# Kernel optimization log

Measured on AMD Instinct MI355X. Metric: run time of the kernel, lower is better.

The kernel has to match this reference:

```python
import jax, jax.numpy as jnp
import numpy as np

D_MODEL = 96
D_INNER = 2 * D_MODEL          # expand=2
D_STATE = 16
D_CONV = 4
DT_RANK = 6                    # ceil(96/16)


def setup_inputs() -> dict:
    key = jax.random.key(0)
    ks = jax.random.split(key, 12)
    B, C, H, W = 4, D_MODEL, 64, 64
    # dt_proj bias init (inverse-softplus of dt sampled log-uniform in [1e-3, 1e-1])
    dtv = jnp.exp(jax.random.uniform(ks[7], (D_INNER,), jnp.float32)
                  * (np.log(0.1) - np.log(0.001)) + np.log(0.001))
    dtv = jnp.clip(dtv, 1e-4, None)
    dt_proj_b = dtv + jnp.log(-jnp.expm1(-dtv))
    dt_std = DT_RANK ** -0.5
    return {
        "x": jax.random.normal(ks[0], (B, C, H, W), jnp.float32),
        "proj_w": jax.random.normal(ks[1], (2 * C, C, 1, 1), jnp.float32) * 0.05,
        "dconv_w": jax.random.normal(ks[2], (C, 2 * C, 3, 3), jnp.float32) * 0.02,
        "in_proj_w": jax.random.normal(ks[3], (2 * D_INNER, C), jnp.float32) * 0.05,
        "conv1d_w": jax.random.normal(ks[4], (D_INNER, D_CONV), jnp.float32) * 0.2,
        "conv1d_b": jnp.zeros((D_INNER,), jnp.float32),
        "x_proj_w": jax.random.normal(ks[5], (DT_RANK + 2 * D_STATE, D_INNER), jnp.float32) * 0.05,
        "dt_proj_w": jax.random.uniform(ks[6], (D_INNER, DT_RANK), jnp.float32, -dt_std, dt_std),
        "dt_proj_b": dt_proj_b,
        "A_log": jnp.log(jnp.tile(jnp.arange(1, D_STATE + 1, dtype=jnp.float32), (D_INNER, 1))),
        "D": jnp.ones((D_INNER,), jnp.float32),
        "out_proj_w": jax.random.normal(ks[8], (C, D_INNER), jnp.float32) * 0.05,
    }


def _cssm_forward(x, proj_w, dconv_w, in_proj_w, conv1d_w, conv1d_b,
                  x_proj_w, dt_proj_w, dt_proj_b, A_log, D, out_proj_w):
    Bsz, Cdim, H, W = x.shape
    L = H * W
    # proj (1x1 conv, no bias) then dconv (3x3 conv, pad 1, no bias)
    xp = jax.lax.conv_general_dilated(x, proj_w, (1, 1), 'VALID',
                                      dimension_numbers=('NCHW', 'OIHW', 'NCHW'))
    xp = jax.lax.conv_general_dilated(xp, dconv_w, (1, 1), ((1, 1), (1, 1)),
                                      dimension_numbers=('NCHW', 'OIHW', 'NCHW'))
    seq = xp.reshape(Bsz, Cdim, L).transpose(0, 2, 1)            # (B, L, C)
    # in_proj (no bias) -> (B, 2*d_inner, L)
    xz = jnp.einsum('blc,ec->bel', seq, in_proj_w)
    xin, z = jnp.split(xz, 2, axis=1)                             # (B, d_inner, L) each
    # causal depthwise conv1d (pad d_conv-1 on left) + SiLU
    xpad = jnp.pad(xin, ((0, 0), (0, 0), (D_CONV - 1, 0)))
    xc = jax.lax.conv_general_dilated(xpad, conv1d_w[:, None, :], (1,), 'VALID',
                                      dimension_numbers=('NCH', 'OIH', 'NCH'),
                                      feature_group_count=D_INNER)
    xc = jax.nn.silu(xc + conv1d_b[None, :, None])                # (B, d_inner, L)
    # x_proj -> dt (rank), B (state), C (state)
    x_dbl = jnp.einsum('bdl,ed->ble', xc, x_proj_w)               # (B, L, rank+2n)
    dt, Bc, Cc = jnp.split(x_dbl, [DT_RANK, DT_RANK + D_STATE], axis=-1)
    delta = jax.nn.softplus(jnp.einsum('blr,dr->bld', dt, dt_proj_w) + dt_proj_b)  # (B,L,d)
    A = -jnp.exp(A_log)                                           # (d, n)
    u = xc.transpose(0, 2, 1)                                     # (B, L, d)
    # selective scan: h_t = exp(delta_t A) * h_{t-1} + delta_t B_t u_t  (diag, per channel/state)
    dA = jnp.exp(delta[..., None] * A)                            # (B,L,d,n)
    dBu = delta[..., None] * Bc[:, :, None, :] * u[..., None]     # (B,L,d,n)

    def combine(c1, c2):
        a1, b1 = c1
        a2, b2 = c2
        return a2 * a1, a2 * b1 + b2

    _, h = jax.lax.associative_scan(combine, (dA, dBu), axis=1)   # (B,L,d,n)
    y = jnp.einsum('bldn,bln->bld', h, Cc) + D * u                # (B,L,d)
    y = y * jax.nn.silu(z.transpose(0, 2, 1))                     # gate
    out = jnp.einsum('bld,cd->blc', y, out_proj_w)                # (B,L,C)
    return out.transpose(0, 2, 1).reshape(Bsz, Cdim, H, W)


def reference(x, proj_w, dconv_w, in_proj_w, conv1d_w, conv1d_b,
              x_proj_w, dt_proj_w, dt_proj_b, A_log, D, out_proj_w):
    return _cssm_forward(x, proj_w, dconv_w, in_proj_w, conv1d_w, conv1d_b,
                         x_proj_w, dt_proj_w, dt_proj_b, A_log, D, out_proj_w)
```

## Files before the change

kernel.cpp:

```cpp
#include <hip/hip_runtime.h>
#include <math.h>

#define LL    4096
#define CDIM  96
#define DIN   192
#define NST   16
#define XE    38

typedef __attribute__((ext_vector_type(8))) short v8s;
typedef __attribute__((ext_vector_type(4))) float v4f;
typedef unsigned short ushort_t;
typedef unsigned int uint_t;

#if __has_builtin(__builtin_amdgcn_exp2f)
__device__ __forceinline__ float fexp2(float x) { return __builtin_amdgcn_exp2f(x); }
#else
__device__ __forceinline__ float fexp2(float x) { return exp2f(x); }
#endif
#if __has_builtin(__builtin_amdgcn_logf)
__device__ __forceinline__ float flog2(float x) { return __builtin_amdgcn_logf(x); }
#else
__device__ __forceinline__ float flog2(float x) { return __log2f(x); }
#endif

__device__ __forceinline__ float siluf(float x) {
    return x * __builtin_amdgcn_rcpf(1.f + fexp2(-1.44269504f * x));
}
__device__ __forceinline__ ushort_t f2bf(float f) {
    uint_t u = __builtin_bit_cast(uint_t, f);
    return (ushort_t)((u + 0x7fffu + ((u >> 16) & 1u)) >> 16);
}
__device__ __forceinline__ float bf2f(ushort_t u) {
    return __builtin_bit_cast(float, (uint_t)u << 16);
}

__global__ __launch_bounds__(256) void k_prep(const float* __restrict__ proj_w,
                                              const float* __restrict__ dconv_w,
                                              const float* __restrict__ in_proj_w,
                                              const float* __restrict__ out_proj_w,
                                              const float* __restrict__ x_proj_w,
                                              const float* __restrict__ x,
                                              ushort_t* __restrict__ Wbf,
                                              ushort_t* __restrict__ Wibf,
                                              ushort_t* __restrict__ Wobf,
                                              ushort_t* __restrict__ Wxbf,
                                              ushort_t* __restrict__ xT) {
    int bid = blockIdx.x;
    if (bid < 576) {
        int i = bid * 256 + threadIdx.x;
        if (i < 82944) {
            int k = i % 9;
            int c = (i / 9) % 96;
            int o = i / 864;
            float s = 0.f;
            for (int j = 0; j < 192; ++j)
                s += dconv_w[(o * 192 + j) * 9 + k] * proj_w[j * 96 + c];
            Wbf[(k * 96 + o) * 96 + c] = f2bf(s);
            return;
        }
        i -= 82944;
        if (i < 36864) { Wibf[i] = f2bf(in_proj_w[i]); return; }
        i -= 36864;
        if (i < 18432) { Wobf[i] = f2bf(out_proj_w[i]); return; }
        i -= 18432;
        if (i < 9216) {
            int e = i / 192;
            Wxbf[i] = (e < XE) ? f2bf(x_proj_w[i]) : (ushort_t)0;
        }
        return;
    }
    int bid2 = bid - 576;
    int yy = bid2 % 66;
    int b  = bid2 / 66;
    int yv = yy - 1;
    for (int i = threadIdx.x; i < 68 * 12; i += 256) {
        int xx = i % 68, cig = i / 68;
        int xv = xx - 1;
        ushort_t u[8];
        if (yv >= 0 && yv < 64 && xv >= 0 && xv < 64) {
            const float* sp = x + ((size_t)(b * 96 + cig * 8)) * LL + yv * 64 + xv;
#pragma unroll
            for (int j = 0; j < 8; ++j) u[j] = f2bf(sp[j * LL]);
        } else {
#pragma unroll
            for (int j = 0; j < 8; ++j) u[j] = 0;
        }
        uint4 pk;
        pk.x = u[0] | ((uint_t)u[1] << 16); pk.y = u[2] | ((uint_t)u[3] << 16);
        pk.z = u[4] | ((uint_t)u[5] << 16); pk.w = u[6] | ((uint_t)u[7] << 16);
        *(uint4*)(xT + (((size_t)b * 66 + yy) * 68 + xx) * 96 + cig * 8) = pk;
    }
}

__global__ __launch_bounds__(384, 2) void k_convin(const ushort_t* __restrict__ xT,
                                                   const ushort_t* __restrict__ Wbf,
                                                   const ushort_t* __restrict__ Wibf,
                                                   ushort_t* __restrict__ xzb) {
    __shared__ ushort_t s_seq[32 * 104];
    int tid = threadIdx.x;
    int w = tid >> 6, l = tid & 63;
    int n = l & 15, g = l >> 4;
    int blk = blockIdx.x;
    int b = blk >> 7, rem = blk & 127;
    int y = rem >> 1, half = rem & 1;
    int lx = (w & 1) * 16;
    int x0 = half * 32 + lx;
    int co0 = (w >> 1) * 32;
    v4f acc0 = {0.f, 0.f, 0.f, 0.f};
    v4f acc1 = {0.f, 0.f, 0.f, 0.f};
    const ushort_t* xb = xT + (((size_t)b * 66 + y) * 68 + x0 + n) * 96 + g * 8;
    const ushort_t* aw = Wbf + ((size_t)co0 + n) * 96 + g * 8;
#pragma unroll
    for (int tap = 0; tap < 9; ++tap) {
        int dy = tap / 3, dx = tap % 3;
        const ushort_t* bp = xb + (dy * 68 + dx) * 96;
        const ushort_t* ap = aw + (size_t)tap * 9216;
#pragma unroll
        for (int kk = 0; kk < 3; ++kk) {
            v8s bf = *(const v8s*)(bp + kk * 32);
            v8s a0 = *(const v8s*)(ap + kk * 32);
            v8s a1 = *(const v8s*)(ap + 1536 + kk * 32);
            acc0 = __builtin_amdgcn_mfma_f32_16x16x32_bf16(a0, bf, acc0, 0, 0, 0);
            acc1 = __builtin_amdgcn_mfma_f32_16x16x32_bf16(a1, bf, acc1, 0, 0, 0);
        }
    }
    {
        int ll = lx + n;
        ushort_t* sp = s_seq + ll * 104 + co0 + g * 4;
        ushort4 p0, p1;
        p0.x = f2bf(acc0[0]); p0.y = f2bf(acc0[1]); p0.z = f2bf(acc0[2]); p0.w = f2bf(acc0[3]);
        p1.x = f2bf(acc1[0]); p1.y = f2bf(acc1[1]); p1.z = f2bf(acc1[2]); p1.w = f2bf(acc1[3]);
        *(ushort4*)sp = p0;
        *(ushort4*)(sp + 16) = p1;
    }
    __syncthreads();
    int coh = w * 64;
    v4f acc[4][2];
#pragma unroll
    for (int mt = 0; mt < 4; ++mt)
#pragma unroll
        for (int lt = 0; lt < 2; ++lt) acc[mt][lt] = (v4f){0.f, 0.f, 0.f, 0.f};
    const ushort_t* ap2 = Wibf + ((size_t)coh + n) * 96 + g * 8;
#pragma unroll
    for (int lt = 0; lt < 2; ++lt) {
        const ushort_t* bp2 = s_seq + (lt * 16 + n) * 104 + g * 8;
#pragma unroll
        for (int kk = 0; kk < 3; ++kk) {
            v8s bf = *(const v8s*)(bp2 + kk * 32);
#pragma unroll
            for (int mt = 0; mt < 4; ++mt) {
                v8s af = *(const v8s*)(ap2 + mt * 16 * 96 + kk * 32);
                acc[mt][lt] = __builtin_amdgcn_mfma_f32_16x16x32_bf16(af, bf, acc[mt][lt], 0, 0, 0);
            }
        }
    }
    int l0g = y * 64 + half * 32;
    ushort_t* ob = xzb + (size_t)b * 384 * LL + l0g + n;
#pragma unroll
    for (int mt = 0; mt < 4; ++mt) {
        int e = coh + mt * 16 + g * 4;
#pragma unroll
        for (int lt = 0; lt < 2; ++lt)
#pragma unroll
            for (int r = 0; r < 4; ++r)
                ob[(size_t)(e + r) * LL + lt * 16] = f2bf(acc[mt][lt][r]);
    }
}

__global__ __launch_bounds__(256) void k_conv1d(const ushort_t* __restrict__ xzb,
                                                const float* __restrict__ w,
                                                const float* __restrict__ bias,
                                                ushort_t* __restrict__ xcT) {
    int tid = threadIdx.x;
    int d_l = tid >> 2, tg = tid & 3;
    int b = blockIdx.z, dg = blockIdx.y, tt = blockIdx.x;
    int d = dg * 64 + d_l;
    int t0 = tt * 16 + tg * 4;
    const ushort_t* xin = xzb + (size_t)(b * 384 + d) * LL;
    ushort4 cu = *(const ushort4*)(xin + t0);
    float pm3 = 0.f, pm2 = 0.f, pm1 = 0.f;
    if (t0 > 0) {
        ushort4 pv = *(const ushort4*)(xin + t0 - 4);
        pm3 = bf2f(pv.y); pm2 = bf2f(pv.z); pm1 = bf2f(pv.w);
    }
    float in[7] = {pm3, pm2, pm1, bf2f(cu.x), bf2f(cu.y), bf2f(cu.z), bf2f(cu.w)};
    float w0 = w[d * 4 + 0], w1 = w[d * 4 + 1], w2 = w[d * 4 + 2], w3 = w[d * 4 + 3];
    float bb = bias[d];
    ushort_t* xt = xcT + ((size_t)b * 4096 + t0) * DIN + d;
#pragma unroll
    for (int i = 0; i < 4; ++i) {
        float s = bb + w0 * in[i] + w1 * in[i + 1] + w2 * in[i + 2] + w3 * in[i + 3];
        xt[(size_t)i * DIN] = f2bf(siluf(s));
    }
}

__global__ __launch_bounds__(256, 4) void k_xprojm(const ushort_t* __restrict__ xcT,
                                                   const ushort_t* __restrict__ Wxbf,
                                                   float* __restrict__ dtT,
                                                   float* __restrict__ BtP,
                                                   float* __restrict__ CtP) {
    int tid = threadIdx.x;
    int w = tid >> 6, l = tid & 63;
    int n = l & 15, g = l >> 4;
    int b = blockIdx.y;
    int l0 = blockIdx.x * 64 + w * 16;
    const ushort_t* bp = xcT + ((size_t)b * 4096 + l0 + n) * 192 + g * 8;
    const ushort_t* ap = Wxbf + (size_t)n * 192 + g * 8;
    v4f acc[3];
#pragma unroll
    for (int m = 0; m < 3; ++m) acc[m] = (v4f){0.f, 0.f, 0.f, 0.f};
#pragma unroll
    for (int kk = 0; kk < 6; ++kk) {
        v8s bf = *(const v8s*)(bp + kk * 32);
#pragma unroll
        for (int m = 0; m < 3; ++m) {
            v8s af = *(const v8s*)(ap + m * 16 * 192 + kk * 32);
            acc[m] = __builtin_amdgcn_mfma_f32_16x16x32_bf16(af, bf, acc[m], 0, 0, 0);
        }
    }
    float* dtb = dtT + (size_t)b * 6 * LL + l0 + n;
    float* Bb = BtP + ((size_t)b * LL + l0 + n) * 16;
    float* Cb = CtP + ((size_t)b * LL + l0 + n) * 16;
#pragma unroll
    for (int m = 0; m < 3; ++m)
#pragma unroll
        for (int r = 0; r < 4; ++r) {
            int e = m * 16 + g * 4 + r;
            float v = acc[m][r];
            if (e < 6)       dtb[(size_t)e * LL] = v;
            else if (e < 22) Bb[e - 6] = v;
            else if (e < 38) Cb[e - 22] = v;
        }
}

__global__ __launch_bounds__(512, 6) void k_scan(const float* __restrict__ dtT,
                                                 const float* __restrict__ dtw,
                                                 const float* __restrict__ dtpb,
                                                 const float* __restrict__ c1w,
                                                 const float* __restrict__ c1b,
                                                 const float* __restrict__ BtP,
                                                 const float* __restrict__ CtP,
                                                 const float* __restrict__ A_log,
                                                 const float* __restrict__ Dp,
                                                 ushort_t* __restrict__ xzb) {
    __shared__ float s_d[32 * 132];
    __shared__ float s_u[32 * 132];
    __shared__ float s_a[32][17];
    __shared__ float s_h[32][17];
    int tid = threadIdx.x;
    int n = tid & 15, cg = tid >> 4;
    int bd = blockIdx.x;
    int d = bd % DIN, b = bd / DIN;
    const ushort_t* xin  = xzb + (size_t)(b * 384 + d) * LL;
    const ushort_t* zrow = xzb + (size_t)(b * 384 + DIN + d) * LL;
    ushort_t* ygr = xzb + (size_t)(b * 384 + d) * LL;
    float A2 = -__expf(A_log[d * NST + n]) * 1.44269504f;
    float Dd = Dp[d];

    {
        int t8 = tid * 8;
        int li = ((t8 >> 7) * 132) + (t8 & 127);
        float ee[11];
        if (t8 > 0) {
            ushort4 pv = *(const ushort4*)(xin + t8 - 4);
            ee[0] = bf2f(pv.y); ee[1] = bf2f(pv.z); ee[2] = bf2f(pv.w);
        } else {
            ee[0] = ee[1] = ee[2] = 0.f;
        }
        v8s cu = *(const v8s*)(xin + t8);
#pragma unroll
        for (int j = 0; j < 8; ++j) ee[3 + j] = bf2f((ushort_t)cu[j]);
        float cw0 = c1w[d * 4], cw1 = c1w[d * 4 + 1], cw2 = c1w[d * 4 + 2], cw3 = c1w[d * 4 + 3];
        float cb = c1b[d];
#pragma unroll
        for (int j = 0; j < 8; ++j) {
            float s = cb + cw0 * ee[j] + cw1 * ee[j + 1] + cw2 * ee[j + 2] + cw3 * ee[j + 3];
            s_u[li + j] = siluf(s);
        }
        const float* dt0 = dtT + (size_t)b * 6 * LL + t8;
        const float* wr = dtw + d * 6;
        float w0 = wr[0], w1 = wr[1], w2 = wr[2], w3 = wr[3], w4 = wr[4], w5 = wr[5];
        float bb = dtpb[d];
        {
            v4f ra[6];
#pragma unroll
            for (int r = 0; r < 6; ++r) ra[r] = *(const v4f*)(dt0 + r * LL);
            v4f spa;
#pragma unroll
            for (int j = 0; j < 4; ++j) {
                float s1 = bb + w0 * ra[0][j] + w1 * ra[1][j] + w2 * ra[2][j]
                              + w3 * ra[3][j] + w4 * ra[4][j] + w5 * ra[5][j];
                spa[j] = 0.69314718f * flog2(1.f + fexp2(s1 * 1.44269504f));
            }
            *(v4f*)&s_d[li] = spa;
        }
        {
            v4f rb[6];
#pragma unroll
            for (int r = 0; r < 6; ++r) rb[r] = *(const v4f*)(dt0 + r * LL + 4);
            v4f spb;
#pragma unroll
            for (int j = 0; j < 4; ++j) {
                float s2 = bb + w0 * rb[0][j] + w1 * rb[1][j] + w2 * rb[2][j]
                              + w3 * rb[3][j] + w4 * rb[4][j] + w5 * rb[5][j];
                spb[j] = 0.69314718f * flog2(1.f + fexp2(s2 * 1.44269504f));
            }
            *(v4f*)&s_d[li + 4] = spb;
        }
    }
    __syncthreads();

    int t0 = cg * 128;
    int lb = cg * 132;
    const float* pB = BtP + ((size_t)b * LL + t0) * 16 + n;
    const float* pC = CtP + ((size_t)b * LL + t0) * 16 + n;

    float h = 0.f, sdu = 0.f;
    float4 du_c = *(float4*)&s_d[lb];
    float4 u_c  = *(float4*)&s_u[lb];
    float B0 = pB[0], B1 = pB[16], B2 = pB[32], B3 = pB[48];
    for (int s = 0; s < 31; ++s) {
        int ln = lb + s * 4 + 4;
        const float* pBn = pB + s * 64 + 64;
        float4 du_n = *(float4*)&s_d[ln];
        float4 u_n  = *(float4*)&s_u[ln];
        float Bn0 = pBn[0], Bn1 = pBn[16], Bn2 = pBn[32], Bn3 = pBn[48];
        float a0 = fexp2(du_c.x * A2), a1 = fexp2(du_c.y * A2);
        float a2 = fexp2(du_c.z * A2), a3 = fexp2(du_c.w * A2);
        h = fmaf(a0, h, (du_c.x * u_c.x) * B0);
        h = fmaf(a1, h, (du_c.y * u_c.y) * B1);
        h = fmaf(a2, h, (du_c.z * u_c.z) * B2);
        h = fmaf(a3, h, (du_c.w * u_c.w) * B3);
        sdu += (du_c.x + du_c.y) + (du_c.z + du_c.w);
        du_c = du_n; u_c = u_n; B0 = Bn0; B1 = Bn1; B2 = Bn2; B3 = Bn3;
    }
    {
        float a0 = fexp2(du_c.x * A2), a1 = fexp2(du_c.y * A2);
        float a2 = fexp2(du_c.z * A2), a3 = fexp2(du_c.w * A2);
        h = fmaf(a0, h, (du_c.x * u_c.x) * B0);
        h = fmaf(a1, h, (du_c.y * u_c.y) * B1);
        h = fmaf(a2, h, (du_c.z * u_c.z) * B2);
        h = fmaf(a3, h, (du_c.w * u_c.w) * B3);
        sdu += (du_c.x + du_c.y) + (du_c.z + du_c.w);
    }
    s_a[cg][n] = fexp2(sdu * A2);
    s_h[cg][n] = h;
    __syncthreads();

    {
        int l = tid & 63, w = tid >> 6;
        int c = l & 31, nn = (w << 1) | (l >> 5);
        float a  = s_a[c][nn];
        float hh = s_h[c][nn];
#pragma unroll
        for (int st = 1; st < 32; st <<= 1) {
            float ap = __shfl_up(a, st, 32);
            float hp = __shfl_up(hh, st, 32);
            bool ok = (c >= st);
            hh = ok ? fmaf(a, hp, hh) : hh;
            a  = ok ? a * ap : a;
        }
        float h0 = __shfl_up(hh, 1, 32);
        if (c == 0) h0 = 0.f;
        s_a[c][nn] = h0;
    }
    __syncthreads();

    h = s_a[cg][n];
    const int j = n & 3;
    const bool e1 = (j == 1), e2 = (j == 2), e3 = (j == 3);
    du_c = *(float4*)&s_d[lb];
    u_c  = *(float4*)&s_u[lb];
    B0 = pB[0]; B1 = pB[16]; B2 = pB[32]; B3 = pB[48];
    float C0 = pC[0], C1 = pC[16], C2 = pC[32], C3 = pC[48];
    ushort4 z_c = *(const ushort4*)(zrow + t0);
    for (int s = 0; s < 32; ++s) {
        float4 du_n, u_n;
        ushort4 z_n;
        float Bn0, Bn1, Bn2, Bn3, Cn0, Cn1, Cn2, Cn3;
        if (s < 31) {
            int ln = lb + s * 4 + 4;
            const float* pBn = pB + s * 64 + 64;
            const float* pCn = pC + s * 64 + 64;
            du_n = *(float4*)&s_d[ln];
            u_n  = *(float4*)&s_u[ln];
            Bn0 = pBn[0]; Bn1 = pBn[16]; Bn2 = pBn[32]; Bn3 = pBn[48];
            Cn0 = pCn[0]; Cn1 = pCn[16]; Cn2 = pCn[32]; Cn3 = pCn[48];
            z_n = *(const ushort4*)(zrow + t0 + s * 4 + 4);
        }
        float a0 = fexp2(du_c.x * A2), a1 = fexp2(du_c.y * A2);
        float a2 = fexp2(du_c.z * A2), a3 = fexp2(du_c.w * A2);
        h = fmaf(a0, h, (du_c.x * u_c.x) * B0); float p0 = h * C0;
        h = fmaf(a1, h, (du_c.y * u_c.y) * B1); float p1 = h * C1;
        h = fmaf(a2, h, (du_c.z * u_c.z) * B2); float p2 = h * C2;
        h = fmaf(a3, h, (du_c.w * u_c.w) * B3); float p3 = h * C3;
        p0 += __shfl_xor(p0, 1); p0 += __shfl_xor(p0, 2);
        p1 += __shfl_xor(p1, 1); p1 += __shfl_xor(p1, 2);
        p2 += __shfl_xor(p2, 1); p2 += __shfl_xor(p2, 2);
        p3 += __shfl_xor(p3, 1); p3 += __shfl_xor(p3, 2);
        float pj = e3 ? p3 : (e2 ? p2 : (e1 ? p1 : p0));
        pj += __shfl_xor(pj, 4); pj += __shfl_xor(pj, 8);
        float uj = e3 ? u_c.w : (e2 ? u_c.z : (e1 ? u_c.y : u_c.x));
        ushort_t zu = e3 ? z_c.w : (e2 ? z_c.z : (e1 ? z_c.y : z_c.x));
        float yj = fmaf(Dd, uj, pj) * siluf(bf2f(zu));
        if (n < 4)
            ygr[t0 + s * 4 + n] = f2bf(yj);
        du_c = du_n; u_c = u_n; z_c = z_n;
        B0 = Bn0; B1 = Bn1; B2 = Bn2; B3 = Bn3;
        C0 = Cn0; C1 = Cn1; C2 = Cn2; C3 = Cn3;
    }
}

__global__ __launch_bounds__(384, 6) void k_outproj(const ushort_t* __restrict__ xzb,
                                                    const ushort_t* __restrict__ Wobf,
                                                    float* __restrict__ out) {
    __shared__ ushort_t s_yg[16][232];
    int tid = threadIdx.x;
    int b = blockIdx.y;
    int l0 = blockIdx.x * 16;
    const ushort_t* ygb = xzb + (size_t)b * 384 * LL;
    if (tid < 96) {
        int q = tid >> 1, o = tid & 1;
        uint4 v[4];
#pragma unroll
        for (int jj = 0; jj < 4; ++jj)
            v[jj] = *(const uint4*)(ygb + (size_t)(q * 4 + jj) * LL + l0 + o * 8);
        const ushort_t* vs = (const ushort_t*)v;
#pragma unroll
        for (int j2 = 0; j2 < 8; ++j2) {
            ushort4 pk;
            pk.x = vs[j2]; pk.y = vs[8 + j2]; pk.z = vs[16 + j2]; pk.w = vs[24 + j2];
            *(ushort4*)&s_yg[o * 8 + j2][q * 4] = pk;
        }
    }
    __syncthreads();
    int w = tid >> 6, l = tid & 63;
    int n = l & 15, g = l >> 4;
    int c0 = w * 16;
    const ushort_t* bp = &s_yg[n][g * 8];
    const ushort_t* ap = Wobf + ((size_t)c0 + n) * 192 + g * 8;
    v4f acc = {0.f, 0.f, 0.f, 0.f};
#pragma unroll
    for (int kk = 0; kk < 6; ++kk) {
        v8s bf = *(const v8s*)(bp + kk * 32);
        v8s af = *(const v8s*)(ap + kk * 32);
        acc = __builtin_amdgcn_mfma_f32_16x16x32_bf16(af, bf, acc, 0, 0, 0);
    }
    float* ob = out + (size_t)b * 96 * LL + l0 + n;
#pragma unroll
    for (int r = 0; r < 4; ++r)
        ob[(size_t)(c0 + g * 4 + r) * LL] = acc[r];
}

extern "C" void kernel_launch(void* const* d_in, const int* in_sizes, int n_in,
                              void* d_out, int out_size, void* d_ws, size_t ws_size,
                              hipStream_t stream) {
    const float* x         = (const float*)d_in[0];
    const float* proj_w    = (const float*)d_in[1];
    const float* dconv_w   = (const float*)d_in[2];
    const float* in_proj_w = (const float*)d_in[3];
    const float* conv1d_w  = (const float*)d_in[4];
    const float* conv1d_b  = (const float*)d_in[5];
    const float* x_proj_w  = (const float*)d_in[6];
    const float* dt_proj_w = (const float*)d_in[7];
    const float* dt_proj_b = (const float*)d_in[8];
    const float* A_log     = (const float*)d_in[9];
    const float* Dp        = (const float*)d_in[10];
    const float* out_proj_w= (const float*)d_in[11];
    float* out = (float*)d_out;
    float* ws  = (float*)d_ws;

    ushort_t* Wbf  = (ushort_t*)ws;
    ushort_t* Wibf = (ushort_t*)(ws + 41472);
    ushort_t* Wobf = (ushort_t*)(ws + 59904);
    ushort_t* Wxbf = (ushort_t*)(ws + 69120);
    ushort_t* xT   = (ushort_t*)(ws + 73728);
    ushort_t* xzb  = (ushort_t*)(ws + 1721856);
    float* dtT  = ws + 4867584;
    float* BtP  = dtT + 98304;
    float* CtP  = BtP + 262144;
    ushort_t* xcT = (ushort_t*)(CtP + 262144);

    k_prep<<<dim3(840), dim3(256), 0, stream>>>(proj_w, dconv_w, in_proj_w, out_proj_w,
                                                x_proj_w, x, Wbf, Wibf, Wobf, Wxbf, xT);
    k_convin<<<dim3(512), dim3(384), 0, stream>>>(xT, Wbf, Wibf, xzb);
    k_conv1d<<<dim3(256, 3, 4), dim3(256), 0, stream>>>(xzb, conv1d_w, conv1d_b, xcT);
    k_xprojm<<<dim3(64, 4), dim3(256), 0, stream>>>(xcT, Wxbf, dtT, BtP, CtP);
    k_scan<<<dim3(768), dim3(512), 0, stream>>>(dtT, dt_proj_w, dt_proj_b,
                                                conv1d_w, conv1d_b, BtP, CtP,
                                                A_log, Dp, xzb);
    k_outproj<<<dim3(256, 4), dim3(384), 0, stream>>>(xzb, Wobf, out);
}
```

Baseline: 115.9 us.

## Fuse causal conv1d into x_proj GEMM and feed scan precomputed conv output

Merges the depthwise conv1d+SiLU kernel with the x_proj MFMA kernel, staging the conv output in shared memory and also writing it row-major so the scan kernel reads it directly instead of recomputing the conv. The prep kernel now stages each dconv output row in LDS and computes the fused proj·dconv weights per output channel with fmaf. This removes one launch, the transposed xcT round trip, and the redundant conv in the scan. In exchange the fused kernel keeps only 192 of 256 threads busy during the conv phase and adds a block barrier.

```diff
diff --git a/kernel.cpp b/kernel.cpp
--- a/kernel.cpp
+++ b/kernel.cpp
@@ -45,20 +45,24 @@
                                               ushort_t* __restrict__ Wobf,
                                               ushort_t* __restrict__ Wxbf,
                                               ushort_t* __restrict__ xT) {
+    __shared__ float s_dc[1728];
     int bid = blockIdx.x;
-    if (bid < 576) {
-        int i = bid * 256 + threadIdx.x;
-        if (i < 82944) {
-            int k = i % 9;
-            int c = (i / 9) % 96;
-            int o = i / 864;
+    if (bid < 96) {
+        int o = bid;
+        for (int i = threadIdx.x; i < 1728; i += 256)
+            s_dc[i] = dconv_w[o * 1728 + i];
+        __syncthreads();
+        for (int u2 = threadIdx.x; u2 < 864; u2 += 256) {
+            int c = u2 % 96, k = u2 / 96;
             float s = 0.f;
-            for (int j = 0; j < 192; ++j)
-                s += dconv_w[(o * 192 + j) * 9 + k] * proj_w[j * 96 + c];
+            for (int j2 = 0; j2 < 192; ++j2)
+                s = fmaf(s_dc[j2 * 9 + k], proj_w[j2 * 96 + c], s);
             Wbf[(k * 96 + o) * 96 + c] = f2bf(s);
-            return;
-        }
-        i -= 82944;
+        }
+        return;
+    }
+    if (bid < 348) {
+        int i = (bid - 96) * 256 + threadIdx.x;
         if (i < 36864) { Wibf[i] = f2bf(in_proj_w[i]); return; }
         i -= 36864;
         if (i < 18432) { Wobf[i] = f2bf(out_proj_w[i]); return; }
@@ -69,7 +73,7 @@
         }
         return;
     }
-    int bid2 = bid - 576;
+    int bid2 = bid - 348;
     int yy = bid2 % 66;
     int b  = bid2 / 66;
     int yv = yy - 1;
@@ -167,77 +171,103 @@
     }
 }
 
-__global__ __launch_bounds__(256) void k_conv1d(const ushort_t* __restrict__ xzb,
-                                                const float* __restrict__ w,
-                                                const float* __restrict__ bias,
-                                                ushort_t* __restrict__ xcT) {
-    int tid = threadIdx.x;
-    int d_l = tid >> 2, tg = tid & 3;
-    int b = blockIdx.z, dg = blockIdx.y, tt = blockIdx.x;
-    int d = dg * 64 + d_l;
-    int t0 = tt * 16 + tg * 4;
-    const ushort_t* xin = xzb + (size_t)(b * 384 + d) * LL;
-    ushort4 cu = *(const ushort4*)(xin + t0);
-    float pm3 = 0.f, pm2 = 0.f, pm1 = 0.f;
-    if (t0 > 0) {
-        ushort4 pv = *(const ushort4*)(xin + t0 - 4);
-        pm3 = bf2f(pv.y); pm2 = bf2f(pv.z); pm1 = bf2f(pv.w);
-    }
-    float in[7] = {pm3, pm2, pm1, bf2f(cu.x), bf2f(cu.y), bf2f(cu.z), bf2f(cu.w)};
-    float w0 = w[d * 4 + 0], w1 = w[d * 4 + 1], w2 = w[d * 4 + 2], w3 = w[d * 4 + 3];
-    float bb = bias[d];
-    ushort_t* xt = xcT + ((size_t)b * 4096 + t0) * DIN + d;
-#pragma unroll
-    for (int i = 0; i < 4; ++i) {
-        float s = bb + w0 * in[i] + w1 * in[i + 1] + w2 * in[i + 2] + w3 * in[i + 3];
-        xt[(size_t)i * DIN] = f2bf(siluf(s));
-    }
-}
-
-__global__ __launch_bounds__(256, 4) void k_xprojm(const ushort_t* __restrict__ xcT,
+__global__ __launch_bounds__(256, 2) void k_convxp(const ushort_t* __restrict__ xzb,
+                                                   const float* __restrict__ c1w,
+                                                   const float* __restrict__ c1b,
                                                    const ushort_t* __restrict__ Wxbf,
+                                                   ushort_t* __restrict__ xcR,
                                                    float* __restrict__ dtT,
                                                    float* __restrict__ BtP,
                                                    float* __restrict__ CtP) {
+    __shared__ ushort_t s_xc[32][200];
     int tid = threadIdx.x;
+    int b = blockIdx.y;
+    int l0 = blockIdx.x * 32;
+    if (tid < 192) {
+        int d = tid;
+        const ushort_t* xin = xzb + (size_t)(b * 384 + d) * LL;
+        float e[35];
+        if (l0 > 0) {
+            v8s pv = *(const v8s*)(xin + l0 - 8);
+            e[0] = bf2f((ushort_t)pv[5]); e[1] = bf2f((ushort_t)pv[6]); e[2] = bf2f((ushort_t)pv[7]);
+        } else {
+            e[0] = e[1] = e[2] = 0.f;
+        }
+#pragma unroll
+        for (int q = 0; q < 4; ++q) {
+            v8s cv = *(const v8s*)(xin + l0 + q * 8);
+#pragma unroll
+            for (int j = 0; j < 8; ++j) e[3 + q * 8 + j] = bf2f((ushort_t)cv[j]);
+        }
+        float w0 = c1w[d * 4], w1 = c1w[d * 4 + 1], w2 = c1w[d * 4 + 2], w3 = c1w[d * 4 + 3];
+        float bb = c1b[d];
+        ushort_t* xr = xcR + (size_t)(b * 192 + d) * LL + l0;
+#pragma unroll
+        for (int q = 0; q < 4; ++q) {
+            v8s ov;
+#pragma unroll
+            for (int j = 0; j < 8; ++j) {
+                int i = q * 8 + j;
+                float s = bb + w0 * e[i] + w1 * e[i + 1] + w2 * e[i + 2] + w3 * e[i + 3];
+                ushort_t uv = f2bf(siluf(s));
+                ov[j] = (short)uv;
+                s_xc[i][d] = uv;
+            }
+            *(v8s*)(xr + q * 8) = ov;
+        }
+    }
+    __syncthreads();
     int w = tid >> 6, l = tid & 63;
     int n = l & 15, g = l >> 4;
-    int b = blockIdx.y;
-    int l0 = blockIdx.x * 64 + w * 16;
-    const ushort_t* bp = xcT + ((size_t)b * 4096 + l0 + n) * 192 + g * 8;
+    int th = w >> 1, ms = w & 1;
+    int lt = th * 16;
+    int t = l0 + lt + n;
     const ushort_t* ap = Wxbf + (size_t)n * 192 + g * 8;
-    v4f acc[3];
-#pragma unroll
-    for (int m = 0; m < 3; ++m) acc[m] = (v4f){0.f, 0.f, 0.f, 0.f};
-#pragma unroll
-    for (int kk = 0; kk < 6; ++kk) {
-        v8s bf = *(const v8s*)(bp + kk * 32);
-#pragma unroll
-        for (int m = 0; m < 3; ++m) {
-            v8s af = *(const v8s*)(ap + m * 16 * 192 + kk * 32);
-            acc[m] = __builtin_amdgcn_mfma_f32_16x16x32_bf16(af, bf, acc[m], 0, 0, 0);
-        }
-    }
-    float* dtb = dtT + (size_t)b * 6 * LL + l0 + n;
-    float* Bb = BtP + ((size_t)b * LL + l0 + n) * 16;
-    float* Cb = CtP + ((size_t)b * LL + l0 + n) * 16;
-#pragma unroll
-    for (int m = 0; m < 3; ++m)
+    float* dtb = dtT + (size_t)b * 6 * LL + t;
+    float* Bb  = BtP + ((size_t)b * LL + t) * 16;
+    float* Cb  = CtP + ((size_t)b * LL + t) * 16;
+    if (ms == 0) {
+        v4f acc0 = {0.f, 0.f, 0.f, 0.f};
+        v4f acc1 = {0.f, 0.f, 0.f, 0.f};
+#pragma unroll
+        for (int kk = 0; kk < 6; ++kk) {
+            v8s bf = *(const v8s*)&s_xc[lt + n][g * 8 + kk * 32];
+            v8s a0 = *(const v8s*)(ap + kk * 32);
+            v8s a1 = *(const v8s*)(ap + 16 * 192 + kk * 32);
+            acc0 = __builtin_amdgcn_mfma_f32_16x16x32_bf16(a0, bf, acc0, 0, 0, 0);
+            acc1 = __builtin_amdgcn_mfma_f32_16x16x32_bf16(a1, bf, acc1, 0, 0, 0);
+        }
 #pragma unroll
         for (int r = 0; r < 4; ++r) {
-            int e = m * 16 + g * 4 + r;
-            float v = acc[m][r];
-            if (e < 6)       dtb[(size_t)e * LL] = v;
-            else if (e < 22) Bb[e - 6] = v;
-            else if (e < 38) Cb[e - 22] = v;
-        }
+            int e0 = g * 4 + r;
+            float v0 = acc0[r];
+            if (e0 < 6) dtb[(size_t)e0 * LL] = v0;
+            else        Bb[e0 - 6] = v0;
+            int e1 = 16 + g * 4 + r;
+            float v1 = acc1[r];
+            if (e1 < 22) Bb[e1 - 6] = v1;
+            else         Cb[e1 - 22] = v1;
+        }
+    } else {
+        v4f acc2 = {0.f, 0.f, 0.f, 0.f};
+#pragma unroll
+        for (int kk = 0; kk < 6; ++kk) {
+            v8s bf = *(const v8s*)&s_xc[lt + n][g * 8 + kk * 32];
+            v8s a2 = *(const v8s*)(ap + 2 * 16 * 192 + kk * 32);
+            acc2 = __builtin_amdgcn_mfma_f32_16x16x32_bf16(a2, bf, acc2, 0, 0, 0);
+        }
+#pragma unroll
+        for (int r = 0; r < 4; ++r) {
+            int e2 = 32 + g * 4 + r;
+            if (e2 < 38) Cb[e2 - 22] = acc2[r];
+        }
+    }
 }
 
 __global__ __launch_bounds__(512, 6) void k_scan(const float* __restrict__ dtT,
                                                  const float* __restrict__ dtw,
                                                  const float* __restrict__ dtpb,
-                                                 const float* __restrict__ c1w,
-                                                 const float* __restrict__ c1b,
+                                                 const ushort_t* __restrict__ xcR,
                                                  const float* __restrict__ BtP,
                                                  const float* __restrict__ CtP,
                                                  const float* __restrict__ A_log,
@@ -251,7 +281,7 @@
     int n = tid & 15, cg = tid >> 4;
     int bd = blockIdx.x;
     int d = bd % DIN, b = bd / DIN;
-    const ushort_t* xin  = xzb + (size_t)(b * 384 + d) * LL;
+    const ushort_t* urow = xcR + (size_t)(b * 192 + d) * LL;
     const ushort_t* zrow = xzb + (size_t)(b * 384 + DIN + d) * LL;
     ushort_t* ygr = xzb + (size_t)(b * 384 + d) * LL;
     float A2 = -__expf(A_log[d * NST + n]) * 1.44269504f;
@@ -260,23 +290,15 @@
     {
         int t8 = tid * 8;
         int li = ((t8 >> 7) * 132) + (t8 & 127);
-        float ee[11];
-        if (t8 > 0) {
-            ushort4 pv = *(const ushort4*)(xin + t8 - 4);
-            ee[0] = bf2f(pv.y); ee[1] = bf2f(pv.z); ee[2] = bf2f(pv.w);
-        } else {
-            ee[0] = ee[1] = ee[2] = 0.f;
-        }
-        v8s cu = *(const v8s*)(xin + t8);
-#pragma unroll
-        for (int j = 0; j < 8; ++j) ee[3 + j] = bf2f((ushort_t)cu[j]);
-        float cw0 = c1w[d * 4], cw1 = c1w[d * 4 + 1], cw2 = c1w[d * 4 + 2], cw3 = c1w[d * 4 + 3];
-        float cb = c1b[d];
-#pragma unroll
-        for (int j = 0; j < 8; ++j) {
-            float s = cb + cw0 * ee[j] + cw1 * ee[j + 1] + cw2 * ee[j + 2] + cw3 * ee[j + 3];
-            s_u[li + j] = siluf(s);
-        }
+        v8s uu = *(const v8s*)(urow + t8);
+        v4f u0, u1;
+#pragma unroll
+        for (int j = 0; j < 4; ++j) {
+            u0[j] = bf2f((ushort_t)uu[j]);
+            u1[j] = bf2f((ushort_t)uu[4 + j]);
+        }
+        *(v4f*)&s_u[li]     = u0;
+        *(v4f*)&s_u[li + 4] = u1;
         const float* dt0 = dtT + (size_t)b * 6 * LL + t8;
         const float* wr = dtw + d * 6;
         float w0 = wr[0], w1 = wr[1], w2 = wr[2], w3 = wr[3], w4 = wr[4], w5 = wr[5];
@@ -479,15 +501,14 @@
     float* dtT  = ws + 4867584;
     float* BtP  = dtT + 98304;
     float* CtP  = BtP + 262144;
-    ushort_t* xcT = (ushort_t*)(CtP + 262144);
-
-    k_prep<<<dim3(840), dim3(256), 0, stream>>>(proj_w, dconv_w, in_proj_w, out_proj_w,
+    ushort_t* xcR = (ushort_t*)(CtP + 262144);
+
+    k_prep<<<dim3(612), dim3(256), 0, stream>>>(proj_w, dconv_w, in_proj_w, out_proj_w,
                                                 x_proj_w, x, Wbf, Wibf, Wobf, Wxbf, xT);
     k_convin<<<dim3(512), dim3(384), 0, stream>>>(xT, Wbf, Wibf, xzb);
-    k_conv1d<<<dim3(256, 3, 4), dim3(256), 0, stream>>>(xzb, conv1d_w, conv1d_b, xcT);
-    k_xprojm<<<dim3(64, 4), dim3(256), 0, stream>>>(xcT, Wxbf, dtT, BtP, CtP);
-    k_scan<<<dim3(768), dim3(512), 0, stream>>>(dtT, dt_proj_w, dt_proj_b,
-                                                conv1d_w, conv1d_b, BtP, CtP,
+    k_convxp<<<dim3(128, 4), dim3(256), 0, stream>>>(xzb, conv1d_w, conv1d_b, Wxbf,
+                                                     xcR, dtT, BtP, CtP);
+    k_scan<<<dim3(768), dim3(512), 0, stream>>>(dtT, dt_proj_w, dt_proj_b, xcR, BtP, CtP,
                                                 A_log, Dp, xzb);
     k_outproj<<<dim3(256, 4), dim3(384), 0, stream>>>(xzb, Wobf, out);
 }
```

Result: no change. 115.7 us (-0.2%).
